# Kernel tuning notes

Hardware: AMD Instinct MI355X
Metric: run time of the kernel (lower is better)

The kernel has to match this reference:

```python
import jax, jax.numpy as jnp
import numpy as np

DIM = 180      # channel dim C
HEADS = 6      # num_heads
WS = 8         # window_size
HIDDEN = int(DIM * 4.0)  # mlp hidden = 720
HEAD_DIM = DIM // HEADS  # 30


def layernorm(x, scale, bias, eps=1e-5):
    m = jnp.mean(x, axis=-1, keepdims=True)
    v = jnp.var(x, axis=-1, keepdims=True)
    return (x - m) * jax.lax.rsqrt(v + eps) * scale + bias


def setup_inputs() -> dict:
    key = jax.random.key(0)
    ks = jax.random.split(key, 16)
    B, H, W = 4, 256, 256
    s = 0.02  # weight init scale for numerical sanity
    return {
        "x": jax.random.normal(ks[0], (B, H * W, DIM), jnp.float32),
        "norm1_scale": jnp.ones((DIM,), jnp.float32),
        "norm1_bias": jnp.zeros((DIM,), jnp.float32),
        "qkv_w": jax.random.normal(ks[1], (DIM, 3 * DIM), jnp.float32) * s,  # [in,out] == torch W.T
        "qkv_b": jax.random.normal(ks[2], (3 * DIM,), jnp.float32) * s,
        "proj_w": jax.random.normal(ks[3], (DIM, DIM), jnp.float32) * s,
        "proj_b": jax.random.normal(ks[4], (DIM,), jnp.float32) * s,
        "norm2_scale": jnp.ones((DIM,), jnp.float32),
        "norm2_bias": jnp.zeros((DIM,), jnp.float32),
        "mlp_w1": jax.random.normal(ks[5], (DIM, HIDDEN), jnp.float32) * s,
        "mlp_b1": jax.random.normal(ks[6], (HIDDEN,), jnp.float32) * s,
        "mlp_w2": jax.random.normal(ks[7], (HIDDEN, DIM), jnp.float32) * s,
        "mlp_b2": jax.random.normal(ks[8], (DIM,), jnp.float32) * s,
        "H": H,
        "W": W,
    }


def reference(x, norm1_scale, norm1_bias, qkv_w, qkv_b, proj_w, proj_b,
              norm2_scale, norm2_bias, mlp_w1, mlp_b1, mlp_w2, mlp_b2, H, W):
    B, L, C = x.shape
    shortcut = x
    h = layernorm(x, norm1_scale, norm1_bias).reshape(B, H, W, C)
    # pad to multiples of window size (no-op when H,W % WS == 0)
    pad_b = (WS - H % WS) % WS
    pad_r = (WS - W % WS) % WS
    h = jnp.pad(h, ((0, 0), (0, pad_b), (0, pad_r), (0, 0)))
    Hp, Wp = H + pad_b, W + pad_r
    # window_partition: (B,Hp,Wp,C) -> (nW*B, WS*WS, C)
    win = h.reshape(B, Hp // WS, WS, Wp // WS, WS, C)
    win = win.transpose(0, 1, 3, 2, 4, 5).reshape(-1, WS * WS, C)
    Bw, N, _ = win.shape
    # fused qkv projection
    qkv = (win @ qkv_w + qkv_b).reshape(Bw, N, 3, HEADS, HEAD_DIM)
    qkv = qkv.transpose(2, 0, 3, 1, 4)  # (3, Bw, heads, N, head_dim)
    q, k, v = qkv[0], qkv[1], qkv[2]
    q = q * (HEAD_DIM ** -0.5)
    attn = jax.nn.softmax(jnp.einsum('bhnd,bhmd->bhnm', q, k), axis=-1)
    o = jnp.einsum('bhnm,bhmd->bhnd', attn, v)
    o = o.transpose(0, 2, 1, 3).reshape(Bw, N, C)
    o = o @ proj_w + proj_b
    # window_reverse: (nW*B, WS*WS, C) -> (B,Hp,Wp,C)
    h = o.reshape(B, Hp // WS, Wp // WS, WS, WS, C)
    h = h.transpose(0, 1, 3, 2, 4, 5).reshape(B, Hp, Wp, C)
    h = h[:, :H, :W, :].reshape(B, H * W, C)
    x = shortcut + h
    # MLP with exact (erf) GELU, matching torch nn.GELU default
    y = layernorm(x, norm2_scale, norm2_bias)
    y = jax.nn.gelu(y @ mlp_w1 + mlp_b1, approximate=False) @ mlp_w2 + mlp_b2
    return x + y
```

## Files before the change

### kernel.cpp

```cpp
#include <hip/hip_runtime.h>

typedef unsigned int u32;
typedef unsigned short u16;
typedef __attribute__((ext_vector_type(8))) __bf16 bf16x8;
typedef __attribute__((ext_vector_type(4))) float f32x4;

#define MFMA(a,b,c) __builtin_amdgcn_mfma_f32_16x16x32_bf16(a,b,c,0,0,0)

__device__ __forceinline__ float bf2f(u16 v){ return __uint_as_float(((u32)v) << 16); }
__device__ __forceinline__ u16 f2bf(float f){
  u32 u = __float_as_uint(f);
  u += 0x7fffu + ((u >> 16) & 1u);
  return (u16)(u >> 16);
}
__device__ __forceinline__ u32 pack2(float a, float b){
  return (u32)f2bf(a) | ((u32)f2bf(b) << 16);
}
__device__ __forceinline__ float gelu_fast(float v){
  float t = v*(-1.5957691216f - 0.0713548163f*v*v);
  return v / (1.f + __expf(t));
}

#define OQKV 0
#define OWP  122880
#define OW1  159744
#define OW2  307200
#define NW_TOT 448512

__global__ void swin_unpack(const float* __restrict__ qkvw, const float* __restrict__ projw,
                            const float* __restrict__ w1, const float* __restrict__ w2,
                            u16* __restrict__ ws){
  int idx = blockIdx.x * 256 + threadIdx.x;
  if (idx >= NW_TOT) return;
  float val = 0.f;
  if (idx < OWP){
    int t = idx, nt = t / 3072, r = t % 3072, kt = r >> 9, e = r & 511;
    int lane = e >> 3, j = e & 7;
    int n = nt*16 + (lane & 15), k = kt*32 + (lane >> 4)*8 + j;
    if (n < 576){
      int p = n / 192, c = n - p*192;
      if (c < 180 && k < 180) val = qkvw[k*540 + p*180 + c];
    }
  } else if (idx < OW1){
    int t = idx - OWP, nt = t / 3072, r = t % 3072, kt = r >> 9, e = r & 511;
    int lane = e >> 3, j = e & 7;
    int n = nt*16 + (lane & 15), k = kt*32 + (lane >> 4)*8 + j;
    if (n < 180 && k < 180) val = projw[k*180 + n];
  } else if (idx < OW2){
    int t = idx - OW1, nt = t / 3072, r = t % 3072, kt = r >> 9, e = r & 511;
    int lane = e >> 3, j = e & 7;
    int n = nt*16 + (lane & 15), k = kt*32 + (lane >> 4)*8 + j;
    if (n < 720 && k < 180) val = w1[k*720 + n];
  } else {
    int t = idx - OW2, nt = t / 11776, r = t % 11776, kt = r >> 9, e = r & 511;
    int lane = e >> 3, j = e & 7;
    int n = nt*16 + (lane & 15), k = kt*32 + (lane >> 4)*8 + j;
    if (n < 180 && k < 720) val = w2[k*180 + n];
  }
  ws[idx] = f2bf(val);
}

#define A_Y   0
#define A_Q   25600
#define A_K   51200
#define A_VT  76800
#define A_P   104448
#define A_RB  122880

__global__ __launch_bounds__(512, 1) void swin_attn(
    const float* __restrict__ x, const float* __restrict__ n1s, const float* __restrict__ n1b,
    const u16* __restrict__ ws, const float* __restrict__ qkvb,
    const float* __restrict__ projb, float* __restrict__ out){
  __shared__ __align__(16) char sm[123136];
  const int tid = threadIdx.x;
  const int w8 = tid >> 6, l = tid & 63, l15 = l & 15, lq = l >> 4;
  const int mh = w8 >> 2, wc = w8 & 3;
  int* rb = (int*)(sm + A_RB);
  const f32x4 fz = {0.f, 0.f, 0.f, 0.f};

  if (tid < 64){
    int wb = blockIdx.x;
    int b = wb >> 10, wy = (wb >> 5) & 31, wx = wb & 31;
    rb[tid] = b*65536 + (wy*8 + (tid>>3))*256 + (wx*8 + (tid&7));
  }
  for (int i = tid; i < 2304; i += 512){
    int row = i / 36, t = i - row*36;
    if (t < 24){
      int buf = (t >= 12) ? A_K : A_Q; int tt = t % 12;
      *(u16*)(sm + buf + row*400 + ((tt>>1)*32 + 30 + (tt&1))*2) = 0;
    } else
      *(u16*)(sm + A_Y + row*400 + (180 + t - 24)*2) = 0;
  }
  __syncthreads();

  {
    int r3 = l & 7, lq2 = l >> 3;
    int n = w8*8 + r3;
    const float4* px = (const float4*)(x + (size_t)rb[n]*180);
    float4 v[6];
    #pragma unroll
    for (int i = 0; i < 5; ++i) v[i] = px[lq2 + 8*i];
    v[5] = (lq2 < 5) ? px[lq2 + 40] : make_float4(0.f,0.f,0.f,0.f);
    float s = 0.f, ss = 0.f;
    #pragma unroll
    for (int i = 0; i < 6; ++i){
      s  += v[i].x + v[i].y + v[i].z + v[i].w;
      ss += v[i].x*v[i].x + v[i].y*v[i].y + v[i].z*v[i].z + v[i].w*v[i].w;
    }
    #pragma unroll
    for (int m = 8; m <= 32; m <<= 1){ s += __shfl_xor(s, m); ss += __shfl_xor(ss, m); }
    float mean = s * (1.f/180.f);
    float rstd = rsqrtf(ss * (1.f/180.f) - mean*mean + 1e-5f);
    u32* yr = (u32*)(sm + A_Y + n*400);
    const float4* s4 = (const float4*)n1s;
    const float4* b4 = (const float4*)n1b;
    #pragma unroll
    for (int i = 0; i < 6; ++i){
      if (i < 5 || lq2 < 5){
        int c4 = lq2 + 8*i;
        float4 sc = s4[c4], bi = b4[c4];
        float e0 = (v[i].x - mean)*rstd*sc.x + bi.x;
        float e1 = (v[i].y - mean)*rstd*sc.y + bi.y;
        float e2 = (v[i].z - mean)*rstd*sc.z + bi.z;
        float e3 = (v[i].w - mean)*rstd*sc.w + bi.w;
        yr[c4*2]     = pack2(e0, e1);
        yr[c4*2 + 1] = pack2(e2, e3);
      }
    }
  }
  __syncthreads();

  {
    const int ntb = w8*5;
    f32x4 acc[4][5];
    #pragma unroll
    for (int m = 0; m < 4; ++m)
      #pragma unroll
      for (int i = 0; i < 5; ++i) acc[m][i] = fz;
    bf16x8 bcur[5];
    #pragma unroll
    for (int i = 0; i < 5; ++i)
      bcur[i] = *(const bf16x8*)(ws + OQKV + ((ntb+i)*6 + 0)*512 + l*8);
    #pragma unroll
    for (int kt = 0; kt < 6; ++kt){
      bf16x8 bnxt[5];
      if (kt < 5){
        #pragma unroll
        for (int i = 0; i < 5; ++i)
          bnxt[i] = *(const bf16x8*)(ws + OQKV + ((ntb+i)*6 + kt + 1)*512 + l*8);
      }
      bf16x8 a[4];
      #pragma unroll
      for (int m = 0; m < 4; ++m)
        a[m] = *(const bf16x8*)(sm + A_Y + (m*16 + l15)*400 + kt*64 + lq*16);
      #pragma unroll
      for (int m = 0; m < 4; ++m)
        #pragma unroll
        for (int i = 0; i < 5; ++i)
          acc[m][i] = MFMA(a[m], bcur[i], acc[m][i]);
      if (kt < 5){
        #pragma unroll
        for (int i = 0; i < 5; ++i) bcur[i] = bnxt[i];
      }
    }
    #pragma unroll
    for (int i = 0; i < 5; ++i){
      int n = (ntb + i)*16 + l15;
      if (n < 576){
        int p = n / 192, c = n - p*192;
        if (c < 180){
          float bias = qkvb[p*180 + c];
          int h = c / 30, d = c - h*30;
          int colp = h*32 + d;
          #pragma unroll
          for (int m = 0; m < 4; ++m)
            #pragma unroll
            for (int r = 0; r < 4; ++r){
              float val = acc[m][i][r] + bias;
              int tok = m*16 + lq*4 + r;
              if (p == 0)      *(u16*)(sm + A_Q + tok*400 + colp*2) = f2bf(val * 0.18257418583505536f);
              else if (p == 1) *(u16*)(sm + A_K + tok*400 + colp*2) = f2bf(val);
              else             *(u16*)(sm + A_VT + colp*144 + tok*2) = f2bf(val);
            }
        }
      }
    }
  }
  __syncthreads();

  {
    const int tq = w8 & 3, hbase = (w8 >> 2)*3;
    for (int h = hbase; h < hbase + 3; ++h){
      bf16x8 aq = *(const bf16x8*)(sm + A_Q + (tq*16 + l15)*400 + h*64 + lq*16);
      f32x4 s[4];
      #pragma unroll
      for (int nt = 0; nt < 4; ++nt){
        bf16x8 bk = *(const bf16x8*)(sm + A_K + (nt*16 + l15)*400 + h*64 + lq*16);
        s[nt] = MFMA(aq, bk, fz);
      }
      #pragma unroll
      for (int r = 0; r < 4; ++r){
        float mx = fmaxf(fmaxf(s[0][r], s[1][r]), fmaxf(s[2][r], s[3][r]));
        mx = fmaxf(mx, __shfl_xor(mx, 1));
        mx = fmaxf(mx, __shfl_xor(mx, 2));
        mx = fmaxf(mx, __shfl_xor(mx, 4));
        mx = fmaxf(mx, __shfl_xor(mx, 8));
        float e0 = __expf(s[0][r]-mx), e1 = __expf(s[1][r]-mx);
        float e2 = __expf(s[2][r]-mx), e3 = __expf(s[3][r]-mx);
        float sum = e0 + e1 + e2 + e3;
        sum += __shfl_xor(sum,1); sum += __shfl_xor(sum,2);
        sum += __shfl_xor(sum,4); sum += __shfl_xor(sum,8);
        float iv = 1.f / sum;
        char* pr = sm + A_P + w8*2304 + (lq*4 + r)*144 + l15*2;
        *(u16*)(pr)      = f2bf(e0 * iv);
        *(u16*)(pr + 32) = f2bf(e1 * iv);
        *(u16*)(pr + 64) = f2bf(e2 * iv);
        *(u16*)(pr + 96) = f2bf(e3 * iv);
      }
      asm volatile("s_waitcnt lgkmcnt(0)" ::: "memory");
      f32x4 o0 = fz, o1 = fz;
      #pragma unroll
      for (int kt = 0; kt < 2; ++kt){
        bf16x8 aP  = *(const bf16x8*)(sm + A_P + w8*2304 + l15*144 + kt*64 + lq*16);
        bf16x8 bv0 = *(const bf16x8*)(sm + A_VT + (h*32 + l15)*144 + kt*64 + lq*16);
        bf16x8 bv1 = *(const bf16x8*)(sm + A_VT + (h*32 + 16 + l15)*144 + kt*64 + lq*16);
        o0 = MFMA(aP, bv0, o0);
        o1 = MFMA(aP, bv1, o1);
      }
      #pragma unroll
      for (int r = 0; r < 4; ++r){
        int tok = tq*16 + lq*4 + r;
        {
          int col = h*30 + l15;
          *(u16*)(sm + A_Y + tok*400 + col*2) = f2bf(o0[r]);
        }
        if (l15 < 14){
          int col = h*30 + 16 + l15;
          *(u16*)(sm + A_Y + tok*400 + col*2) = f2bf(o1[r]);
        }
      }
    }
  }
  __syncthreads();

  {
    f32x4 acc[2][3];
    #pragma unroll
    for (int m = 0; m < 2; ++m)
      #pragma unroll
      for (int i = 0; i < 3; ++i) acc[m][i] = fz;
    bf16x8 bcur[3];
    #pragma unroll
    for (int i = 0; i < 3; ++i)
      bcur[i] = *(const bf16x8*)(ws + OWP + ((wc*3+i)*6 + 0)*512 + l*8);
    #pragma unroll
    for (int kt = 0; kt < 6; ++kt){
      bf16x8 bnxt[3];
      int ktn = (kt < 5) ? kt + 1 : kt;
      #pragma unroll
      for (int i = 0; i < 3; ++i)
        bnxt[i] = *(const bf16x8*)(ws + OWP + ((wc*3+i)*6 + ktn)*512 + l*8);
      bf16x8 ah[2];
      #pragma unroll
      for (int m = 0; m < 2; ++m)
        ah[m] = *(const bf16x8*)(sm + A_Y + (mh*32 + m*16 + l15)*400 + kt*64 + lq*16);
      #pragma unroll
      for (int m = 0; m < 2; ++m)
        #pragma unroll
        for (int i = 0; i < 3; ++i)
          acc[m][i] = MFMA(ah[m], bcur[i], acc[m][i]);
      #pragma unroll
      for (int i = 0; i < 3; ++i) bcur[i] = bnxt[i];
    }
    float* res = (float*)(sm + A_Q);
    #pragma unroll
    for (int i = 0; i < 3; ++i){
      int col = (wc*3 + i)*16 + l15;
      if (col < 180){
        float bias = projb[col];
        #pragma unroll
        for (int m = 0; m < 2; ++m)
          #pragma unroll
          for (int r = 0; r < 4; ++r)
            res[(mh*32 + m*16 + lq*4 + r)*180 + col] = acc[m][i][r] + bias;
      }
    }
  }
  __syncthreads();

  {
    const float4* res4 = (const float4*)(sm + A_Q);
    for (int idx = tid; idx < 2880; idx += 512){
      int n = idx / 45, c4 = idx - n*45;
      size_t g4 = (size_t)rb[n]*45 + c4;
      float4 rv = res4[idx];
      float4 xv = ((const float4*)x)[g4];
      float4 o; o.x = rv.x + xv.x; o.y = rv.y + xv.y; o.z = rv.z + xv.z; o.w = rv.w + xv.w;
      ((float4*)out)[g4] = o;
    }
  }
}

#define M_Y 0
#define M_G 25600

__global__ __launch_bounds__(512, 1) void swin_mlp(
    const float* __restrict__ n2s, const float* __restrict__ n2b,
    const u16* __restrict__ ws, const float* __restrict__ b1, const float* __restrict__ b2,
    float* __restrict__ out){
  __shared__ __align__(16) char sm[124928];
  const int tid = threadIdx.x;
  const int w8 = tid >> 6, l = tid & 63, l15 = l & 15, lq = l >> 4;
  const size_t base = (size_t)blockIdx.x * (64*180);
  const f32x4 fz = {0.f, 0.f, 0.f, 0.f};

  for (int i = tid; i < 768; i += 512){
    int row = i / 12, col = 180 + i % 12;
    *(u16*)(sm + M_Y + row*400 + col*2) = 0;
  }
  {
    int r3 = l & 7, lq2 = l >> 3;
    int n = w8*8 + r3;
    const float4* px = (const float4*)(out + base + (size_t)n*180);
    float4 v[6];
    #pragma unroll
    for (int i = 0; i < 5; ++i) v[i] = px[lq2 + 8*i];
    v[5] = (lq2 < 5) ? px[lq2 + 40] : make_float4(0.f,0.f,0.f,0.f);
    float s = 0.f, ss = 0.f;
    #pragma unroll
    for (int i = 0; i < 6; ++i){
      s  += v[i].x + v[i].y + v[i].z + v[i].w;
      ss += v[i].x*v[i].x + v[i].y*v[i].y + v[i].z*v[i].z + v[i].w*v[i].w;
    }
    #pragma unroll
    for (int m = 8; m <= 32; m <<= 1){ s += __shfl_xor(s, m); ss += __shfl_xor(ss, m); }
    float mean = s * (1.f/180.f);
    float rstd = rsqrtf(ss * (1.f/180.f) - mean*mean + 1e-5f);
    u32* yr = (u32*)(sm + M_Y + n*400);
    const float4* s4 = (const float4*)n2s;
    const float4* b4 = (const float4*)n2b;
    #pragma unroll
    for (int i = 0; i < 6; ++i){
      if (i < 5 || lq2 < 5){
        int c4 = lq2 + 8*i;
        float4 sc = s4[c4], bi = b4[c4];
        float e0 = (v[i].x - mean)*rstd*sc.x + bi.x;
        float e1 = (v[i].y - mean)*rstd*sc.y + bi.y;
        float e2 = (v[i].z - mean)*rstd*sc.z + bi.z;
        float e3 = (v[i].w - mean)*rstd*sc.w + bi.w;
        yr[c4*2]     = pack2(e0, e1);
        yr[c4*2 + 1] = pack2(e2, e3);
      }
    }
  }
  __syncthreads();

  for (int ch = 0; ch < 2; ++ch){
    const int ntb = w8*6 + ch*3;
    f32x4 acc[4][3];
    #pragma unroll
    for (int m = 0; m < 4; ++m)
      #pragma unroll
      for (int i = 0; i < 3; ++i) acc[m][i] = fz;
    bf16x8 wb0[3], wb1[3];
    #pragma unroll
    for (int i = 0; i < 3; ++i){
      wb0[i] = *(const bf16x8*)(ws + OW1 + ((ntb+i)*6 + 0)*512 + l*8);
      wb1[i] = *(const bf16x8*)(ws + OW1 + ((ntb+i)*6 + 1)*512 + l*8);
    }
    #pragma unroll
    for (int kt = 0; kt < 6; ++kt){
      bf16x8 wbn[3];
      if (kt + 2 < 6){
        #pragma unroll
        for (int i = 0; i < 3; ++i)
          wbn[i] = *(const bf16x8*)(ws + OW1 + ((ntb+i)*6 + kt + 2)*512 + l*8);
      }
      bf16x8 a[4];
      #pragma unroll
      for (int m = 0; m < 4; ++m)
        a[m] = *(const bf16x8*)(sm + M_Y + (m*16 + l15)*400 + kt*64 + lq*16);
      #pragma unroll
      for (int m = 0; m < 4; ++m)
        #pragma unroll
        for (int i = 0; i < 3; ++i)
          acc[m][i] = MFMA(a[m], wb0[i], acc[m][i]);
      #pragma unroll
      for (int i = 0; i < 3; ++i){ wb0[i] = wb1[i]; if (kt + 2 < 6) wb1[i] = wbn[i]; }
    }
    #pragma unroll
    for (int i = 0; i < 3; ++i){
      int gc = (ntb + i)*16 + l15;
      float bias = (gc < 720) ? b1[gc] : 0.f;
      #pragma unroll
      for (int m = 0; m < 4; ++m)
        #pragma unroll
        for (int r = 0; r < 4; ++r){
          float v = acc[m][i][r] + bias;
          float gel = (gc < 720) ? gelu_fast(v) : 0.f;
          *(u16*)(sm + M_G + (m*16 + lq*4 + r)*1552 + gc*2) = f2bf(gel);
        }
    }
  }
  __syncthreads();

  {
    const int mh2 = w8 >> 2, wc4 = w8 & 3;
    f32x4 acc2[2][3];
    #pragma unroll
    for (int m = 0; m < 2; ++m)
      #pragma unroll
      for (int i = 0; i < 3; ++i) acc2[m][i] = fz;
    bf16x8 wb0[3], wb1[3];
    #pragma unroll
    for (int i = 0; i < 3; ++i){
      wb0[i] = *(const bf16x8*)(ws + OW2 + ((wc4*3+i)*23 + 0)*512 + l*8);
      wb1[i] = *(const bf16x8*)(ws + OW2 + ((wc4*3+i)*23 + 1)*512 + l*8);
    }
    for (int kt = 0; kt < 23; ++kt){
      bf16x8 wbn[3];
      int ktn = (kt < 21) ? kt + 2 : 22;
      #pragma unroll
      for (int i = 0; i < 3; ++i)
        wbn[i] = *(const bf16x8*)(ws + OW2 + ((wc4*3+i)*23 + ktn)*512 + l*8);
      bf16x8 a[2];
      #pragma unroll
      for (int m = 0; m < 2; ++m)
        a[m] = *(const bf16x8*)(sm + M_G + (mh2*32 + m*16 + l15)*1552 + kt*64 + lq*16);
      #pragma unroll
      for (int m = 0; m < 2; ++m)
        #pragma unroll
        for (int i = 0; i < 3; ++i)
          acc2[m][i] = MFMA(a[m], wb0[i], acc2[m][i]);
      #pragma unroll
      for (int i = 0; i < 3; ++i){ wb0[i] = wb1[i]; wb1[i] = wbn[i]; }
    }
    __syncthreads();

    float* res = (float*)(sm + M_G);
    #pragma unroll
    for (int i = 0; i < 3; ++i){
      int col = (wc4*3 + i)*16 + l15;
      if (col < 180){
        float bias = b2[col];
        #pragma unroll
        for (int m = 0; m < 2; ++m)
          #pragma unroll
          for (int r = 0; r < 4; ++r)
            res[(mh2*32 + m*16 + lq*4 + r)*180 + col] = acc2[m][i][r] + bias;
      }
    }
  }
  __syncthreads();

  {
    const float4* res4 = (const float4*)(sm + M_G);
    float4* og = (float4*)(out + base);
    for (int idx = tid; idx < 2880; idx += 512){
      float4 rv = res4[idx];
      float4 xv = og[idx];
      float4 o; o.x = rv.x + xv.x; o.y = rv.y + xv.y; o.z = rv.z + xv.z; o.w = rv.w + xv.w;
      og[idx] = o;
    }
  }
}

extern "C" void kernel_launch(void* const* d_in, const int* in_sizes, int n_in,
                              void* d_out, int out_size, void* d_ws, size_t ws_size,
                              hipStream_t stream){
  const float* x     = (const float*)d_in[0];
  const float* n1s   = (const float*)d_in[1];
  const float* n1b   = (const float*)d_in[2];
  const float* qkvw  = (const float*)d_in[3];
  const float* qkvb  = (const float*)d_in[4];
  const float* projw = (const float*)d_in[5];
  const float* projb = (const float*)d_in[6];
  const float* n2s   = (const float*)d_in[7];
  const float* n2b   = (const float*)d_in[8];
  const float* w1    = (const float*)d_in[9];
  const float* b1    = (const float*)d_in[10];
  const float* w2    = (const float*)d_in[11];
  const float* b2    = (const float*)d_in[12];
  float* outp = (float*)d_out;
  u16* wsp = (u16*)d_ws;

  swin_unpack<<<(NW_TOT + 255) / 256, 256, 0, stream>>>(qkvw, projw, w1, w2, wsp);
  swin_attn<<<4096, 512, 0, stream>>>(x, n1s, n1b, wsp, qkvb, projb, outp);
  swin_mlp<<<4096, 512, 0, stream>>>(n2s, n2b, wsp, b1, b2, outp);
}
```

Before: 696.7 us.

## Fuse attention and MLP into one kernel with chunked hidden-dim pipeline

Merges the attention and MLP kernels into a single kernel. The attention residual stays in shared memory, and LayerNorm2 plus both MLP GEMMs run on the same 64-token window. This removes the global write and re-read of the intermediate activations. The 720-wide hidden layer is processed in three 256-column chunks, each computed then consumed by the second GEMM, so the fused kernel fits the existing shared-memory budget. The cost is extra barriers per chunk, and the final output is written as scattered strided scalar stores rather than float4.

```diff
diff --git a/kernel.cpp b/kernel.cpp
--- a/kernel.cpp
+++ b/kernel.cpp
@@ -66,11 +66,14 @@
 #define A_VT  76800
 #define A_P   104448
 #define A_RB  122880
-
-__global__ __launch_bounds__(512, 1) void swin_attn(
+#define A_G   76800
+
+__global__ __launch_bounds__(512, 1) void swin_fused(
     const float* __restrict__ x, const float* __restrict__ n1s, const float* __restrict__ n1b,
-    const u16* __restrict__ ws, const float* __restrict__ qkvb,
-    const float* __restrict__ projb, float* __restrict__ out){
+    const u16* __restrict__ ws, const float* __restrict__ qkvb, const float* __restrict__ projb,
+    const float* __restrict__ n2s, const float* __restrict__ n2b,
+    const float* __restrict__ b1, const float* __restrict__ b2,
+    float* __restrict__ out){
   __shared__ __align__(16) char sm[123136];
   const int tid = threadIdx.x;
   const int w8 = tid >> 6, l = tid & 63, l15 = l & 15, lq = l >> 4;
@@ -289,39 +292,22 @@
   __syncthreads();
 
   {
-    const float4* res4 = (const float4*)(sm + A_Q);
+    float4* res4 = (float4*)(sm + A_Q);
     for (int idx = tid; idx < 2880; idx += 512){
       int n = idx / 45, c4 = idx - n*45;
       size_t g4 = (size_t)rb[n]*45 + c4;
       float4 rv = res4[idx];
       float4 xv = ((const float4*)x)[g4];
       float4 o; o.x = rv.x + xv.x; o.y = rv.y + xv.y; o.z = rv.z + xv.z; o.w = rv.w + xv.w;
-      ((float4*)out)[g4] = o;
-    }
-  }
-}
-
-#define M_Y 0
-#define M_G 25600
-
-__global__ __launch_bounds__(512, 1) void swin_mlp(
-    const float* __restrict__ n2s, const float* __restrict__ n2b,
-    const u16* __restrict__ ws, const float* __restrict__ b1, const float* __restrict__ b2,
-    float* __restrict__ out){
-  __shared__ __align__(16) char sm[124928];
-  const int tid = threadIdx.x;
-  const int w8 = tid >> 6, l = tid & 63, l15 = l & 15, lq = l >> 4;
-  const size_t base = (size_t)blockIdx.x * (64*180);
-  const f32x4 fz = {0.f, 0.f, 0.f, 0.f};
-
-  for (int i = tid; i < 768; i += 512){
-    int row = i / 12, col = 180 + i % 12;
-    *(u16*)(sm + M_Y + row*400 + col*2) = 0;
-  }
+      res4[idx] = o;
+    }
+  }
+  __syncthreads();
+
   {
     int r3 = l & 7, lq2 = l >> 3;
     int n = w8*8 + r3;
-    const float4* px = (const float4*)(out + base + (size_t)n*180);
+    const float4* px = (const float4*)(sm + A_Q) + n*45;
     float4 v[6];
     #pragma unroll
     for (int i = 0; i < 5; ++i) v[i] = px[lq2 + 8*i];
@@ -336,7 +322,7 @@
     for (int m = 8; m <= 32; m <<= 1){ s += __shfl_xor(s, m); ss += __shfl_xor(ss, m); }
     float mean = s * (1.f/180.f);
     float rstd = rsqrtf(ss * (1.f/180.f) - mean*mean + 1e-5f);
-    u32* yr = (u32*)(sm + M_Y + n*400);
+    u32* yr = (u32*)(sm + A_Y + n*400);
     const float4* s4 = (const float4*)n2s;
     const float4* b4 = (const float4*)n2b;
     #pragma unroll
@@ -355,55 +341,6 @@
   }
   __syncthreads();
 
-  for (int ch = 0; ch < 2; ++ch){
-    const int ntb = w8*6 + ch*3;
-    f32x4 acc[4][3];
-    #pragma unroll
-    for (int m = 0; m < 4; ++m)
-      #pragma unroll
-      for (int i = 0; i < 3; ++i) acc[m][i] = fz;
-    bf16x8 wb0[3], wb1[3];
-    #pragma unroll
-    for (int i = 0; i < 3; ++i){
-      wb0[i] = *(const bf16x8*)(ws + OW1 + ((ntb+i)*6 + 0)*512 + l*8);
-      wb1[i] = *(const bf16x8*)(ws + OW1 + ((ntb+i)*6 + 1)*512 + l*8);
-    }
-    #pragma unroll
-    for (int kt = 0; kt < 6; ++kt){
-      bf16x8 wbn[3];
-      if (kt + 2 < 6){
-        #pragma unroll
-        for (int i = 0; i < 3; ++i)
-          wbn[i] = *(const bf16x8*)(ws + OW1 + ((ntb+i)*6 + kt + 2)*512 + l*8);
-      }
-      bf16x8 a[4];
-      #pragma unroll
-      for (int m = 0; m < 4; ++m)
-        a[m] = *(const bf16x8*)(sm + M_Y + (m*16 + l15)*400 + kt*64 + lq*16);
-      #pragma unroll
-      for (int m = 0; m < 4; ++m)
-        #pragma unroll
-        for (int i = 0; i < 3; ++i)
-          acc[m][i] = MFMA(a[m], wb0[i], acc[m][i]);
-      #pragma unroll
-      for (int i = 0; i < 3; ++i){ wb0[i] = wb1[i]; if (kt + 2 < 6) wb1[i] = wbn[i]; }
-    }
-    #pragma unroll
-    for (int i = 0; i < 3; ++i){
-      int gc = (ntb + i)*16 + l15;
-      float bias = (gc < 720) ? b1[gc] : 0.f;
-      #pragma unroll
-      for (int m = 0; m < 4; ++m)
-        #pragma unroll
-        for (int r = 0; r < 4; ++r){
-          float v = acc[m][i][r] + bias;
-          float gel = (gc < 720) ? gelu_fast(v) : 0.f;
-          *(u16*)(sm + M_G + (m*16 + lq*4 + r)*1552 + gc*2) = f2bf(gel);
-        }
-    }
-  }
-  __syncthreads();
-
   {
     const int mh2 = w8 >> 2, wc4 = w8 & 3;
     f32x4 acc2[2][3];
@@ -411,33 +348,77 @@
     for (int m = 0; m < 2; ++m)
       #pragma unroll
       for (int i = 0; i < 3; ++i) acc2[m][i] = fz;
-    bf16x8 wb0[3], wb1[3];
-    #pragma unroll
-    for (int i = 0; i < 3; ++i){
-      wb0[i] = *(const bf16x8*)(ws + OW2 + ((wc4*3+i)*23 + 0)*512 + l*8);
-      wb1[i] = *(const bf16x8*)(ws + OW2 + ((wc4*3+i)*23 + 1)*512 + l*8);
-    }
-    for (int kt = 0; kt < 23; ++kt){
-      bf16x8 wbn[3];
-      int ktn = (kt < 21) ? kt + 2 : 22;
-      #pragma unroll
-      for (int i = 0; i < 3; ++i)
-        wbn[i] = *(const bf16x8*)(ws + OW2 + ((wc4*3+i)*23 + ktn)*512 + l*8);
-      bf16x8 a[2];
-      #pragma unroll
-      for (int m = 0; m < 2; ++m)
-        a[m] = *(const bf16x8*)(sm + M_G + (mh2*32 + m*16 + l15)*1552 + kt*64 + lq*16);
-      #pragma unroll
-      for (int m = 0; m < 2; ++m)
+
+    for (int c = 0; c < 3; ++c){
+      f32x4 acc1[4][2];
+      #pragma unroll
+      for (int m = 0; m < 4; ++m)
+        #pragma unroll
+        for (int i = 0; i < 2; ++i) acc1[m][i] = fz;
+      const int gnt = c*16 + w8*2;
+      bf16x8 wb[2];
+      #pragma unroll
+      for (int i = 0; i < 2; ++i)
+        wb[i] = *(const bf16x8*)(ws + OW1 + ((gnt+i)*6 + 0)*512 + l*8);
+      #pragma unroll
+      for (int kt = 0; kt < 6; ++kt){
+        bf16x8 wn[2];
+        if (kt < 5){
+          #pragma unroll
+          for (int i = 0; i < 2; ++i)
+            wn[i] = *(const bf16x8*)(ws + OW1 + ((gnt+i)*6 + kt + 1)*512 + l*8);
+        }
+        bf16x8 a[4];
+        #pragma unroll
+        for (int m = 0; m < 4; ++m)
+          a[m] = *(const bf16x8*)(sm + A_Y + (m*16 + l15)*400 + kt*64 + lq*16);
+        #pragma unroll
+        for (int m = 0; m < 4; ++m)
+          #pragma unroll
+          for (int i = 0; i < 2; ++i)
+            acc1[m][i] = MFMA(a[m], wb[i], acc1[m][i]);
+        if (kt < 5){
+          #pragma unroll
+          for (int i = 0; i < 2; ++i) wb[i] = wn[i];
+        }
+      }
+      #pragma unroll
+      for (int i = 0; i < 2; ++i){
+        int colc = w8*32 + i*16 + l15;
+        int gc = c*256 + colc;
+        float bias = (gc < 720) ? b1[gc] : 0.f;
+        #pragma unroll
+        for (int m = 0; m < 4; ++m)
+          #pragma unroll
+          for (int r = 0; r < 4; ++r){
+            float v = acc1[m][i][r] + bias;
+            float gel = (gc < 720) ? gelu_fast(v) : 0.f;
+            *(u16*)(sm + A_G + (m*16 + lq*4 + r)*520 + colc*2) = f2bf(gel);
+          }
+      }
+      __syncthreads();
+
+      const int nkt = (c == 2) ? 7 : 8;
+      for (int ktl = 0; ktl < nkt; ++ktl){
+        int ktg = c*8 + ktl;
+        bf16x8 wb2[3];
         #pragma unroll
         for (int i = 0; i < 3; ++i)
-          acc2[m][i] = MFMA(a[m], wb0[i], acc2[m][i]);
-      #pragma unroll
-      for (int i = 0; i < 3; ++i){ wb0[i] = wb1[i]; wb1[i] = wbn[i]; }
-    }
-    __syncthreads();
-
-    float* res = (float*)(sm + M_G);
+          wb2[i] = *(const bf16x8*)(ws + OW2 + ((wc4*3+i)*23 + ktg)*512 + l*8);
+        bf16x8 a2[2];
+        #pragma unroll
+        for (int m = 0; m < 2; ++m)
+          a2[m] = *(const bf16x8*)(sm + A_G + (mh2*32 + m*16 + l15)*520 + ktl*64 + lq*16);
+        #pragma unroll
+        for (int m = 0; m < 2; ++m)
+          #pragma unroll
+          for (int i = 0; i < 3; ++i)
+            acc2[m][i] = MFMA(a2[m], wb2[i], acc2[m][i]);
+      }
+      if (c < 2) __syncthreads();
+    }
+
+    const float* x2 = (const float*)(sm + A_Q);
     #pragma unroll
     for (int i = 0; i < 3; ++i){
       int col = (wc4*3 + i)*16 + l15;
@@ -446,21 +427,11 @@
         #pragma unroll
         for (int m = 0; m < 2; ++m)
           #pragma unroll
-          for (int r = 0; r < 4; ++r)
-            res[(mh2*32 + m*16 + lq*4 + r)*180 + col] = acc2[m][i][r] + bias;
-      }
-    }
-  }
-  __syncthreads();
-
-  {
-    const float4* res4 = (const float4*)(sm + M_G);
-    float4* og = (float4*)(out + base);
-    for (int idx = tid; idx < 2880; idx += 512){
-      float4 rv = res4[idx];
-      float4 xv = og[idx];
-      float4 o; o.x = rv.x + xv.x; o.y = rv.y + xv.y; o.z = rv.z + xv.z; o.w = rv.w + xv.w;
-      og[idx] = o;
+          for (int r = 0; r < 4; ++r){
+            int tok = mh2*32 + m*16 + lq*4 + r;
+            out[(size_t)rb[tok]*180 + col] = x2[tok*180 + col] + acc2[m][i][r] + bias;
+          }
+      }
     }
   }
 }
@@ -485,6 +456,5 @@
   u16* wsp = (u16*)d_ws;
 
   swin_unpack<<<(NW_TOT + 255) / 256, 256, 0, stream>>>(qkvw, projw, w1, w2, wsp);
-  swin_attn<<<4096, 512, 0, stream>>>(x, n1s, n1b, wsp, qkvb, projb, outp);
-  swin_mlp<<<4096, 512, 0, stream>>>(n2s, n2b, wsp, b1, b2, outp);
-}
+  swin_fused<<<4096, 512, 0, stream>>>(x, n1s, n1b, wsp, qkvb, projb, n2s, n2b, b1, b2, outp);
+}
```

Result: slower. 795.5 us (+14.2%).

## Raise attention and MLP kernels to 12 waves per block with rebalanced tiles

Applied to the files above, without the earlier changes.

Both fused kernels now launch 768 threads (12 wavefronts) instead of 512. The QKV, attention-head, projection, fc1 and fc2 tile assignments are redistributed so each wave owns fewer output tiles, and the per-wave softmax scratch area in LDS grows to 12 slots. The goal is more resident waves per CU to hide LDS and global-load latency, with smaller per-wave register footprints. The cost is more LDS (about 132 KB for attention) and some idle waves in the LayerNorm phases.

```diff
diff --git a/kernel.cpp b/kernel.cpp
--- a/kernel.cpp
+++ b/kernel.cpp
@@ -65,16 +65,15 @@
 #define A_K   51200
 #define A_VT  76800
 #define A_P   104448
-#define A_RB  122880
-
-__global__ __launch_bounds__(512, 1) void swin_attn(
+#define A_RB  132096
+
+__global__ __launch_bounds__(768, 1) void swin_attn(
     const float* __restrict__ x, const float* __restrict__ n1s, const float* __restrict__ n1b,
     const u16* __restrict__ ws, const float* __restrict__ qkvb,
     const float* __restrict__ projb, float* __restrict__ out){
-  __shared__ __align__(16) char sm[123136];
+  __shared__ __align__(16) char sm[132352];
   const int tid = threadIdx.x;
-  const int w8 = tid >> 6, l = tid & 63, l15 = l & 15, lq = l >> 4;
-  const int mh = w8 >> 2, wc = w8 & 3;
+  const int w12 = tid >> 6, l = tid & 63, l15 = l & 15, lq = l >> 4;
   int* rb = (int*)(sm + A_RB);
   const f32x4 fz = {0.f, 0.f, 0.f, 0.f};
 
@@ -83,7 +82,7 @@
     int b = wb >> 10, wy = (wb >> 5) & 31, wx = wb & 31;
     rb[tid] = b*65536 + (wy*8 + (tid>>3))*256 + (wx*8 + (tid&7));
   }
-  for (int i = tid; i < 2304; i += 512){
+  for (int i = tid; i < 2304; i += 768){
     int row = i / 36, t = i - row*36;
     if (t < 24){
       int buf = (t >= 12) ? A_K : A_Q; int tt = t % 12;
@@ -93,9 +92,9 @@
   }
   __syncthreads();
 
-  {
+  if (w12 < 8){
     int r3 = l & 7, lq2 = l >> 3;
-    int n = w8*8 + r3;
+    int n = w12*8 + r3;
     const float4* px = (const float4*)(x + (size_t)rb[n]*180);
     float4 v[6];
     #pragma unroll
@@ -131,22 +130,22 @@
   __syncthreads();
 
   {
-    const int ntb = w8*5;
-    f32x4 acc[4][5];
+    const int ntb = w12*3;
+    f32x4 acc[4][3];
     #pragma unroll
     for (int m = 0; m < 4; ++m)
       #pragma unroll
-      for (int i = 0; i < 5; ++i) acc[m][i] = fz;
-    bf16x8 bcur[5];
-    #pragma unroll
-    for (int i = 0; i < 5; ++i)
+      for (int i = 0; i < 3; ++i) acc[m][i] = fz;
+    bf16x8 bcur[3];
+    #pragma unroll
+    for (int i = 0; i < 3; ++i)
       bcur[i] = *(const bf16x8*)(ws + OQKV + ((ntb+i)*6 + 0)*512 + l*8);
     #pragma unroll
     for (int kt = 0; kt < 6; ++kt){
-      bf16x8 bnxt[5];
+      bf16x8 bnxt[3];
       if (kt < 5){
         #pragma unroll
-        for (int i = 0; i < 5; ++i)
+        for (int i = 0; i < 3; ++i)
           bnxt[i] = *(const bf16x8*)(ws + OQKV + ((ntb+i)*6 + kt + 1)*512 + l*8);
       }
       bf16x8 a[4];
@@ -156,41 +155,39 @@
       #pragma unroll
       for (int m = 0; m < 4; ++m)
         #pragma unroll
-        for (int i = 0; i < 5; ++i)
+        for (int i = 0; i < 3; ++i)
           acc[m][i] = MFMA(a[m], bcur[i], acc[m][i]);
       if (kt < 5){
         #pragma unroll
-        for (int i = 0; i < 5; ++i) bcur[i] = bnxt[i];
-      }
-    }
-    #pragma unroll
-    for (int i = 0; i < 5; ++i){
+        for (int i = 0; i < 3; ++i) bcur[i] = bnxt[i];
+      }
+    }
+    #pragma unroll
+    for (int i = 0; i < 3; ++i){
       int n = (ntb + i)*16 + l15;
-      if (n < 576){
-        int p = n / 192, c = n - p*192;
-        if (c < 180){
-          float bias = qkvb[p*180 + c];
-          int h = c / 30, d = c - h*30;
-          int colp = h*32 + d;
+      int p = n / 192, c = n - p*192;
+      if (c < 180){
+        float bias = qkvb[p*180 + c];
+        int h = c / 30, d = c - h*30;
+        int colp = h*32 + d;
+        #pragma unroll
+        for (int m = 0; m < 4; ++m)
           #pragma unroll
-          for (int m = 0; m < 4; ++m)
-            #pragma unroll
-            for (int r = 0; r < 4; ++r){
-              float val = acc[m][i][r] + bias;
-              int tok = m*16 + lq*4 + r;
-              if (p == 0)      *(u16*)(sm + A_Q + tok*400 + colp*2) = f2bf(val * 0.18257418583505536f);
-              else if (p == 1) *(u16*)(sm + A_K + tok*400 + colp*2) = f2bf(val);
-              else             *(u16*)(sm + A_VT + colp*144 + tok*2) = f2bf(val);
-            }
-        }
-      }
-    }
-  }
-  __syncthreads();
-
-  {
-    const int tq = w8 & 3, hbase = (w8 >> 2)*3;
-    for (int h = hbase; h < hbase + 3; ++h){
+          for (int r = 0; r < 4; ++r){
+            float val = acc[m][i][r] + bias;
+            int tok = m*16 + lq*4 + r;
+            if (p == 0)      *(u16*)(sm + A_Q + tok*400 + colp*2) = f2bf(val * 0.18257418583505536f);
+            else if (p == 1) *(u16*)(sm + A_K + tok*400 + colp*2) = f2bf(val);
+            else             *(u16*)(sm + A_VT + colp*144 + tok*2) = f2bf(val);
+          }
+      }
+    }
+  }
+  __syncthreads();
+
+  {
+    const int tq = w12 & 3, hbase = (w12 >> 2)*2;
+    for (int h = hbase; h < hbase + 2; ++h){
       bf16x8 aq = *(const bf16x8*)(sm + A_Q + (tq*16 + l15)*400 + h*64 + lq*16);
       f32x4 s[4];
       #pragma unroll
@@ -211,7 +208,7 @@
         sum += __shfl_xor(sum,1); sum += __shfl_xor(sum,2);
         sum += __shfl_xor(sum,4); sum += __shfl_xor(sum,8);
         float iv = 1.f / sum;
-        char* pr = sm + A_P + w8*2304 + (lq*4 + r)*144 + l15*2;
+        char* pr = sm + A_P + w12*2304 + (lq*4 + r)*144 + l15*2;
         *(u16*)(pr)      = f2bf(e0 * iv);
         *(u16*)(pr + 32) = f2bf(e1 * iv);
         *(u16*)(pr + 64) = f2bf(e2 * iv);
@@ -221,7 +218,7 @@
       f32x4 o0 = fz, o1 = fz;
       #pragma unroll
       for (int kt = 0; kt < 2; ++kt){
-        bf16x8 aP  = *(const bf16x8*)(sm + A_P + w8*2304 + l15*144 + kt*64 + lq*16);
+        bf16x8 aP  = *(const bf16x8*)(sm + A_P + w12*2304 + l15*144 + kt*64 + lq*16);
         bf16x8 bv0 = *(const bf16x8*)(sm + A_VT + (h*32 + l15)*144 + kt*64 + lq*16);
         bf16x8 bv1 = *(const bf16x8*)(sm + A_VT + (h*32 + 16 + l15)*144 + kt*64 + lq*16);
         o0 = MFMA(aP, bv0, o0);
@@ -244,45 +241,49 @@
   __syncthreads();
 
   {
-    f32x4 acc[2][3];
+    const int mh2 = w12 / 6, ng6 = w12 % 6;
+    f32x4 acc[2][2];
     #pragma unroll
     for (int m = 0; m < 2; ++m)
       #pragma unroll
-      for (int i = 0; i < 3; ++i) acc[m][i] = fz;
-    bf16x8 bcur[3];
-    #pragma unroll
-    for (int i = 0; i < 3; ++i)
-      bcur[i] = *(const bf16x8*)(ws + OWP + ((wc*3+i)*6 + 0)*512 + l*8);
+      for (int i = 0; i < 2; ++i) acc[m][i] = fz;
+    bf16x8 bcur[2];
+    #pragma unroll
+    for (int i = 0; i < 2; ++i)
+      bcur[i] = *(const bf16x8*)(ws + OWP + ((ng6*2+i)*6 + 0)*512 + l*8);
     #pragma unroll
     for (int kt = 0; kt < 6; ++kt){
-      bf16x8 bnxt[3];
-      int ktn = (kt < 5) ? kt + 1 : kt;
-      #pragma unroll
-      for (int i = 0; i < 3; ++i)
-        bnxt[i] = *(const bf16x8*)(ws + OWP + ((wc*3+i)*6 + ktn)*512 + l*8);
+      bf16x8 bnxt[2];
+      if (kt < 5){
+        #pragma unroll
+        for (int i = 0; i < 2; ++i)
+          bnxt[i] = *(const bf16x8*)(ws + OWP + ((ng6*2+i)*6 + kt + 1)*512 + l*8);
+      }
       bf16x8 ah[2];
       #pragma unroll
       for (int m = 0; m < 2; ++m)
-        ah[m] = *(const bf16x8*)(sm + A_Y + (mh*32 + m*16 + l15)*400 + kt*64 + lq*16);
+        ah[m] = *(const bf16x8*)(sm + A_Y + (mh2*32 + m*16 + l15)*400 + kt*64 + lq*16);
       #pragma unroll
       for (int m = 0; m < 2; ++m)
         #pragma unroll
-        for (int i = 0; i < 3; ++i)
+        for (int i = 0; i < 2; ++i)
           acc[m][i] = MFMA(ah[m], bcur[i], acc[m][i]);
-      #pragma unroll
-      for (int i = 0; i < 3; ++i) bcur[i] = bnxt[i];
+      if (kt < 5){
+        #pragma unroll
+        for (int i = 0; i < 2; ++i) bcur[i] = bnxt[i];
+      }
     }
     float* res = (float*)(sm + A_Q);
     #pragma unroll
-    for (int i = 0; i < 3; ++i){
-      int col = (wc*3 + i)*16 + l15;
+    for (int i = 0; i < 2; ++i){
+      int col = (ng6*2 + i)*16 + l15;
       if (col < 180){
         float bias = projb[col];
         #pragma unroll
         for (int m = 0; m < 2; ++m)
           #pragma unroll
           for (int r = 0; r < 4; ++r)
-            res[(mh*32 + m*16 + lq*4 + r)*180 + col] = acc[m][i][r] + bias;
+            res[(mh2*32 + m*16 + lq*4 + r)*180 + col] = acc[m][i][r] + bias;
       }
     }
   }
@@ -290,7 +291,7 @@
 
   {
     const float4* res4 = (const float4*)(sm + A_Q);
-    for (int idx = tid; idx < 2880; idx += 512){
+    for (int idx = tid; idx < 2880; idx += 768){
       int n = idx / 45, c4 = idx - n*45;
       size_t g4 = (size_t)rb[n]*45 + c4;
       float4 rv = res4[idx];
@@ -304,23 +305,23 @@
 #define M_Y 0
 #define M_G 25600
 
-__global__ __launch_bounds__(512, 1) void swin_mlp(
+__global__ __launch_bounds__(768, 1) void swin_mlp(
     const float* __restrict__ n2s, const float* __restrict__ n2b,
     const u16* __restrict__ ws, const float* __restrict__ b1, const float* __restrict__ b2,
     float* __restrict__ out){
   __shared__ __align__(16) char sm[124928];
   const int tid = threadIdx.x;
-  const int w8 = tid >> 6, l = tid & 63, l15 = l & 15, lq = l >> 4;
+  const int w12 = tid >> 6, l = tid & 63, l15 = l & 15, lq = l >> 4;
   const size_t base = (size_t)blockIdx.x * (64*180);
   const f32x4 fz = {0.f, 0.f, 0.f, 0.f};
 
-  for (int i = tid; i < 768; i += 512){
+  for (int i = tid; i < 768; i += 768){
     int row = i / 12, col = 180 + i % 12;
     *(u16*)(sm + M_Y + row*400 + col*2) = 0;
   }
-  {
+  if (w12 < 8){
     int r3 = l & 7, lq2 = l >> 3;
-    int n = w8*8 + r3;
+    int n = w12*8 + r3;
     const float4* px = (const float4*)(out + base + (size_t)n*180);
     float4 v[6];
     #pragma unroll
@@ -356,24 +357,24 @@
   __syncthreads();
 
   for (int ch = 0; ch < 2; ++ch){
-    const int ntb = w8*6 + ch*3;
-    f32x4 acc[4][3];
+    const int ntb = w12*4 + ch*2;
+    f32x4 acc[4][2];
     #pragma unroll
     for (int m = 0; m < 4; ++m)
       #pragma unroll
-      for (int i = 0; i < 3; ++i) acc[m][i] = fz;
-    bf16x8 wb0[3], wb1[3];
-    #pragma unroll
-    for (int i = 0; i < 3; ++i){
+      for (int i = 0; i < 2; ++i) acc[m][i] = fz;
+    bf16x8 wb0[2], wb1[2];
+    #pragma unroll
+    for (int i = 0; i < 2; ++i){
       wb0[i] = *(const bf16x8*)(ws + OW1 + ((ntb+i)*6 + 0)*512 + l*8);
       wb1[i] = *(const bf16x8*)(ws + OW1 + ((ntb+i)*6 + 1)*512 + l*8);
     }
     #pragma unroll
     for (int kt = 0; kt < 6; ++kt){
-      bf16x8 wbn[3];
+      bf16x8 wbn[2];
       if (kt + 2 < 6){
         #pragma unroll
-        for (int i = 0; i < 3; ++i)
+        for (int i = 0; i < 2; ++i)
           wbn[i] = *(const bf16x8*)(ws + OW1 + ((ntb+i)*6 + kt + 2)*512 + l*8);
       }
       bf16x8 a[4];
@@ -383,13 +384,13 @@
       #pragma unroll
       for (int m = 0; m < 4; ++m)
         #pragma unroll
-        for (int i = 0; i < 3; ++i)
+        for (int i = 0; i < 2; ++i)
           acc[m][i] = MFMA(a[m], wb0[i], acc[m][i]);
       #pragma unroll
-      for (int i = 0; i < 3; ++i){ wb0[i] = wb1[i]; if (kt + 2 < 6) wb1[i] = wbn[i]; }
-    }
-    #pragma unroll
-    for (int i = 0; i < 3; ++i){
+      for (int i = 0; i < 2; ++i){ wb0[i] = wb1[i]; if (kt + 2 < 6) wb1[i] = wbn[i]; }
+    }
+    #pragma unroll
+    for (int i = 0; i < 2; ++i){
       int gc = (ntb + i)*16 + l15;
       float bias = (gc < 720) ? b1[gc] : 0.f;
       #pragma unroll
@@ -405,24 +406,24 @@
   __syncthreads();
 
   {
-    const int mh2 = w8 >> 2, wc4 = w8 & 3;
-    f32x4 acc2[2][3];
+    const int mh2 = w12 / 6, ng6 = w12 % 6;
+    f32x4 acc2[2][2];
     #pragma unroll
     for (int m = 0; m < 2; ++m)
       #pragma unroll
-      for (int i = 0; i < 3; ++i) acc2[m][i] = fz;
-    bf16x8 wb0[3], wb1[3];
-    #pragma unroll
-    for (int i = 0; i < 3; ++i){
-      wb0[i] = *(const bf16x8*)(ws + OW2 + ((wc4*3+i)*23 + 0)*512 + l*8);
-      wb1[i] = *(const bf16x8*)(ws + OW2 + ((wc4*3+i)*23 + 1)*512 + l*8);
+      for (int i = 0; i < 2; ++i) acc2[m][i] = fz;
+    bf16x8 wb0[2], wb1[2];
+    #pragma unroll
+    for (int i = 0; i < 2; ++i){
+      wb0[i] = *(const bf16x8*)(ws + OW2 + ((ng6*2+i)*23 + 0)*512 + l*8);
+      wb1[i] = *(const bf16x8*)(ws + OW2 + ((ng6*2+i)*23 + 1)*512 + l*8);
     }
     for (int kt = 0; kt < 23; ++kt){
-      bf16x8 wbn[3];
+      bf16x8 wbn[2];
       int ktn = (kt < 21) ? kt + 2 : 22;
       #pragma unroll
-      for (int i = 0; i < 3; ++i)
-        wbn[i] = *(const bf16x8*)(ws + OW2 + ((wc4*3+i)*23 + ktn)*512 + l*8);
+      for (int i = 0; i < 2; ++i)
+        wbn[i] = *(const bf16x8*)(ws + OW2 + ((ng6*2+i)*23 + ktn)*512 + l*8);
       bf16x8 a[2];
       #pragma unroll
       for (int m = 0; m < 2; ++m)
@@ -430,17 +431,17 @@
       #pragma unroll
       for (int m = 0; m < 2; ++m)
         #pragma unroll
-        for (int i = 0; i < 3; ++i)
+        for (int i = 0; i < 2; ++i)
           acc2[m][i] = MFMA(a[m], wb0[i], acc2[m][i]);
       #pragma unroll
-      for (int i = 0; i < 3; ++i){ wb0[i] = wb1[i]; wb1[i] = wbn[i]; }
+      for (int i = 0; i < 2; ++i){ wb0[i] = wb1[i]; wb1[i] = wbn[i]; }
     }
     __syncthreads();
 
     float* res = (float*)(sm + M_G);
     #pragma unroll
-    for (int i = 0; i < 3; ++i){
-      int col = (wc4*3 + i)*16 + l15;
+    for (int i = 0; i < 2; ++i){
+      int col = (ng6*2 + i)*16 + l15;
       if (col < 180){
         float bias = b2[col];
         #pragma unroll
@@ -456,7 +457,7 @@
   {
     const float4* res4 = (const float4*)(sm + M_G);
     float4* og = (float4*)(out + base);
-    for (int idx = tid; idx < 2880; idx += 512){
+    for (int idx = tid; idx < 2880; idx += 768){
       float4 rv = res4[idx];
       float4 xv = og[idx];
       float4 o; o.x = rv.x + xv.x; o.y = rv.y + xv.y; o.z = rv.z + xv.z; o.w = rv.w + xv.w;
@@ -485,6 +486,6 @@
   u16* wsp = (u16*)d_ws;
 
   swin_unpack<<<(NW_TOT + 255) / 256, 256, 0, stream>>>(qkvw, projw, w1, w2, wsp);
-  swin_attn<<<4096, 512, 0, stream>>>(x, n1s, n1b, wsp, qkvb, projb, outp);
-  swin_mlp<<<4096, 512, 0, stream>>>(n2s, n2b, wsp, b1, b2, outp);
-}
+  swin_attn<<<4096, 768, 0, stream>>>(x, n1s, n1b, wsp, qkvb, projb, outp);
+  swin_mlp<<<4096, 768, 0, stream>>>(n2s, n2b, wsp, b1, b2, outp);
+}
```

After: 616.0 us, median of 2. -11.6%, faster.
